# Kernel tuning notes

Hardware: AMD Instinct MI355X
Metric: run time of the kernel (lower is better)

The kernel has to match this reference:

```python
import jax, jax.numpy as jnp
import numpy as np

# MAML backbone parameter shapes (standard 4-conv few-shot net + 5-way logits head)
PARAM_SHAPES = [(64, 3, 3, 3), (64,), (64, 64, 3, 3), (64,), (64, 64, 3, 3), (64,),
                (64, 64, 3, 3), (64,), (5, 1600), (5,)]
GATE_DIM = 512   # hierarchicalClustering.input_dim + hidden_dim
B = 256          # meta-batch of tasks (vectorized over the original python loop)


def setup_inputs() -> dict:
    key = jax.random.key(0)
    ks = jax.random.split(key, 1 + 3 * len(PARAM_SHAPES))
    inp = {"emb": jax.random.normal(ks[0], (B, GATE_DIM), dtype=jnp.float32)}
    for i, s in enumerate(PARAM_SHAPES):
        n = int(np.prod(s))
        inp[f"p{i}"] = jax.random.normal(ks[1 + 3 * i], s, dtype=jnp.float32) * 0.05
        inp[f"W{i}"] = jax.random.normal(ks[2 + 3 * i], (n, GATE_DIM), dtype=jnp.float32) / np.float32(np.sqrt(GATE_DIM))
        inp[f"b{i}"] = jnp.zeros((n,), dtype=jnp.float32)
    return inp


def reference(emb, p0, W0, b0, p1, W1, b1, p2, W2, b2, p3, W3, b3, p4, W4, b4,
              p5, W5, b5, p6, W6, b6, p7, W7, b7, p8, W8, b8, p9, W9, b9):
    # Per MAML parameter tensor: eta = sigmoid(Linear(emb)); adapted = eta * theta.
    # Loop is over a small fixed set of structurally distinct params (10), vectorized over tasks B.
    triples = [(p0, W0, b0), (p1, W1, b1), (p2, W2, b2), (p3, W3, b3), (p4, W4, b4),
               (p5, W5, b5), (p6, W6, b6), (p7, W7, b7), (p8, W8, b8), (p9, W9, b9)]
    outs = []
    for p, W, b in triples:
        eta = jax.nn.sigmoid(emb @ W.T + b)          # [B, numel_i]
        outs.append(eta * p.reshape(-1))             # adapted theta_i, flattened
    return jnp.concatenate(outs, axis=1)             # [B, total_numel]
```

## Files before the change

kernel.cpp:

```cpp
#include <hip/hip_runtime.h>
#include <hip/hip_bf16.h>

#define GATE 512
#define MROWS 256
#define NTOT 120581

typedef __attribute__((ext_vector_type(8))) short short8;
typedef __attribute__((ext_vector_type(4))) float  f32x4;

struct GemmParams {
    const float* W[10];
    const float* p[10];
    const float* bias[10];
};

__device__ __forceinline__ short bf16bits(float x) {
    __hip_bfloat16 h = __float2bfloat16(x);
    return *reinterpret_cast<short*>(&h);
}

__global__ void emb_to_bf16(const float* __restrict__ emb,
                            unsigned short* __restrict__ o) {
    int i = (blockIdx.x * blockDim.x + threadIdx.x) * 8;
    f32x4 a = *(const f32x4*)(emb + i);
    f32x4 b = *(const f32x4*)(emb + i + 4);
    short8 r;
#pragma unroll
    for (int j = 0; j < 4; ++j) { r[j] = bf16bits(a[j]); r[4 + j] = bf16bits(b[j]); }
    *(short8*)(o + i) = r;
}

__global__ __launch_bounds__(256, 4) void gate_gemm(GemmParams P,
                                                    const unsigned short* __restrict__ embw,
                                                    float* __restrict__ out)
{
    constexpr int kStarts[11] = {0, 1728, 1792, 38656, 38720, 75584,
                                 75648, 112512, 112576, 120576, 120581};
    __shared__ unsigned short Atile[2][MROWS * 32];

    const int t    = threadIdx.x;
    const int lane = t & 63;
    const int wave = t >> 6;
    const int lr   = lane & 15;
    const int lg   = lane >> 4;

    const int  n     = blockIdx.x * 64 + wave * 16 + lr;
    const bool valid = n < NTOT;
    const int  nc    = valid ? n : NTOT - 1;
    int tt = 0;
#pragma unroll
    for (int i = 1; i < 10; ++i) tt += (nc >= kStarts[i]);
    const int rr = nc - kStarts[tt];
    const float* wrow = P.W[tt] + (size_t)rr * GATE + lg * 8;
    const float pv = P.p[tt][rr];
    const float bv = P.bias[tt][rr];

    const int srow  = t >> 2;
    const int sslot = (t & 3) ^ ((t >> 3) & 3);
    const unsigned short* asrc = embw + (size_t)srow * GATE + sslot * 8;

    const int aslot = lg ^ ((lr >> 1) & 3);
    const int abase = lr * 32 + aslot * 8;

    f32x4 acc[16];
#pragma unroll
    for (int i = 0; i < 16; ++i) acc[i] = (f32x4){0.f, 0.f, 0.f, 0.f};

    auto stage = [&](int buf, int kb) {
#pragma unroll
        for (int i = 0; i < 4; ++i) {
            const unsigned short* src = asrc + (size_t)i * 64 * GATE + kb;
            unsigned short* dst = &Atile[buf][(size_t)(i * 256 + t) * 8];
            __builtin_amdgcn_global_load_lds(
                (const __attribute__((address_space(1))) void*)src,
                (__attribute__((address_space(3))) void*)dst, 16, 0, 0);
        }
    };

    stage(0, 0);
    f32x4 b0 = *(const f32x4*)(wrow);
    f32x4 b1 = *(const f32x4*)(wrow + 4);
    __syncthreads();

    int buf = 0;
#pragma unroll
    for (int ks = 0; ks < 16; ++ks) {
        f32x4 nb0, nb1;
        if (ks < 15) {
            stage(buf ^ 1, (ks + 1) * 32);
            nb0 = *(const f32x4*)(wrow + (ks + 1) * 32);
            nb1 = *(const f32x4*)(wrow + (ks + 1) * 32 + 4);
        }

        short8 bfrag;
#pragma unroll
        for (int j = 0; j < 4; ++j) {
            bfrag[j]     = bf16bits(b0[j]);
            bfrag[4 + j] = bf16bits(b1[j]);
        }

        const unsigned short* ab = &Atile[buf][abase];
#pragma unroll
        for (int mf = 0; mf < 16; ++mf) {
            short8 afrag = *(const short8*)(ab + mf * 512);
            acc[mf] = __builtin_amdgcn_mfma_f32_16x16x32_bf16(afrag, bfrag, acc[mf], 0, 0, 0);
        }

        __syncthreads();
        b0 = nb0; b1 = nb1;
        buf ^= 1;
    }

    if (valid) {
        float* ocol = out + n;
#pragma unroll
        for (int mf = 0; mf < 16; ++mf) {
            const int m0 = mf * 16 + lg * 4;
#pragma unroll
            for (int q = 0; q < 4; ++q) {
                float x   = acc[mf][q] + bv;
                float e   = __expf(-x);
                float eta = __builtin_amdgcn_rcpf(1.0f + e);
                ocol[(size_t)(m0 + q) * NTOT] = eta * pv;
            }
        }
    }
}

extern "C" void kernel_launch(void* const* d_in, const int* in_sizes, int n_in,
                              void* d_out, int out_size, void* d_ws, size_t ws_size,
                              hipStream_t stream) {
    const float* emb = (const float*)d_in[0];
    GemmParams P;
    for (int i = 0; i < 10; ++i) {
        P.p[i]    = (const float*)d_in[1 + 3 * i];
        P.W[i]    = (const float*)d_in[2 + 3 * i];
        P.bias[i] = (const float*)d_in[3 + 3 * i];
    }

    unsigned short* embw = (unsigned short*)d_ws;
    emb_to_bf16<<<(MROWS * GATE) / (256 * 8), 256, 0, stream>>>(emb, embw);

    int nblocks = (NTOT + 63) / 64;
    gate_gemm<<<nblocks, 256, 0, stream>>>(P, embw, (float*)d_out);
}
```

Baseline: 131.3 us.

## Tile waves 2x2 over M and N and stage K in 64-wide phases

Each wave now computes 128 rows by 32 columns instead of 256 rows by 16 columns. Every A fragment loaded from LDS feeds two MFMAs, which halves LDS reads per MFMA. The A staging loads a 64-wide K slab (two 32-wide sub-tiles) per phase with two barriers per phase, instead of double-buffering every 32-wide K step. The trade-off is that global-to-LDS loads are no longer overlapped with compute, since each phase waits at barriers after staging, and each wave now loads two W rows at a time.

```diff
diff --git a/kernel.cpp b/kernel.cpp
--- a/kernel.cpp
+++ b/kernel.cpp
@@ -36,92 +36,126 @@
 {
     constexpr int kStarts[11] = {0, 1728, 1792, 38656, 38720, 75584,
                                  75648, 112512, 112576, 120576, 120581};
-    __shared__ unsigned short Atile[2][MROWS * 32];
+    __shared__ unsigned short Atile[2][MROWS][32];
 
     const int t    = threadIdx.x;
     const int lane = t & 63;
     const int wave = t >> 6;
+    const int wm   = wave >> 1;
+    const int wn   = wave & 1;
     const int lr   = lane & 15;
     const int lg   = lane >> 4;
 
-    const int  n     = blockIdx.x * 64 + wave * 16 + lr;
-    const bool valid = n < NTOT;
-    const int  nc    = valid ? n : NTOT - 1;
-    int tt = 0;
+    const float* wrow[2];
+    float pv[2], bv[2];
+    bool  valid[2];
+    int   ncol[2];
 #pragma unroll
-    for (int i = 1; i < 10; ++i) tt += (nc >= kStarts[i]);
-    const int rr = nc - kStarts[tt];
-    const float* wrow = P.W[tt] + (size_t)rr * GATE + lg * 8;
-    const float pv = P.p[tt][rr];
-    const float bv = P.bias[tt][rr];
+    for (int nf = 0; nf < 2; ++nf) {
+        int n  = blockIdx.x * 64 + wn * 32 + nf * 16 + lr;
+        ncol[nf]  = n;
+        valid[nf] = n < NTOT;
+        int nc = valid[nf] ? n : NTOT - 1;
+        int tt = 0;
+#pragma unroll
+        for (int i = 1; i < 10; ++i) tt += (nc >= kStarts[i]);
+        int r = nc - kStarts[tt];
+        wrow[nf] = P.W[tt] + (size_t)r * GATE + lg * 8;
+        pv[nf]   = P.p[tt][r];
+        bv[nf]   = P.bias[tt][r];
+    }
 
-    const int srow  = t >> 2;
+    const int srow0 = t >> 2;
     const int sslot = (t & 3) ^ ((t >> 3) & 3);
-    const unsigned short* asrc = embw + (size_t)srow * GATE + sslot * 8;
+    const unsigned short* asrc = embw + (size_t)srow0 * GATE + sslot * 8;
+    unsigned short* sdst = &Atile[0][0][0] + (size_t)t * 8;
+
+    auto stage = [&](int ph) {
+#pragma unroll
+        for (int sub = 0; sub < 2; ++sub)
+#pragma unroll
+            for (int i = 0; i < 4; ++i) {
+                const unsigned short* src = asrc + (size_t)i * 64 * GATE + ph * 64 + sub * 32;
+                unsigned short* dst = sdst + sub * 8192 + i * 2048;
+                __builtin_amdgcn_global_load_lds(
+                    (const __attribute__((address_space(1))) void*)src,
+                    (__attribute__((address_space(3))) void*)dst, 16, 0, 0);
+            }
+    };
 
     const int aslot = lg ^ ((lr >> 1) & 3);
-    const int abase = lr * 32 + aslot * 8;
+    const int abase = (wm * 128 + lr) * 32 + aslot * 8;
 
-    f32x4 acc[16];
+    f32x4 acc[8][2];
 #pragma unroll
-    for (int i = 0; i < 16; ++i) acc[i] = (f32x4){0.f, 0.f, 0.f, 0.f};
+    for (int i = 0; i < 8; ++i)
+#pragma unroll
+        for (int j = 0; j < 2; ++j) acc[i][j] = (f32x4){0.f, 0.f, 0.f, 0.f};
 
-    auto stage = [&](int buf, int kb) {
+    f32x4 Bcur[2][2], Bnxt[2][2];
+    auto loadB = [&](f32x4 (&B)[2][2], int gks) {
 #pragma unroll
-        for (int i = 0; i < 4; ++i) {
-            const unsigned short* src = asrc + (size_t)i * 64 * GATE + kb;
-            unsigned short* dst = &Atile[buf][(size_t)(i * 256 + t) * 8];
-            __builtin_amdgcn_global_load_lds(
-                (const __attribute__((address_space(1))) void*)src,
-                (__attribute__((address_space(3))) void*)dst, 16, 0, 0);
+        for (int nf = 0; nf < 2; ++nf) {
+            B[nf][0] = *(const f32x4*)(wrow[nf] + gks * 32);
+            B[nf][1] = *(const f32x4*)(wrow[nf] + gks * 32 + 4);
         }
     };
 
-    stage(0, 0);
-    f32x4 b0 = *(const f32x4*)(wrow);
-    f32x4 b1 = *(const f32x4*)(wrow + 4);
+    stage(0);
+    loadB(Bcur, 0);
     __syncthreads();
 
-    int buf = 0;
+    for (int ph = 0; ph < 8; ++ph) {
 #pragma unroll
-    for (int ks = 0; ks < 16; ++ks) {
-        f32x4 nb0, nb1;
-        if (ks < 15) {
-            stage(buf ^ 1, (ks + 1) * 32);
-            nb0 = *(const f32x4*)(wrow + (ks + 1) * 32);
-            nb1 = *(const f32x4*)(wrow + (ks + 1) * 32 + 4);
+        for (int sub = 0; sub < 2; ++sub) {
+            const int gks = ph * 2 + sub;
+            if (gks < 15) loadB(Bnxt, gks + 1);
+
+            short8 bfrag[2];
+#pragma unroll
+            for (int nf = 0; nf < 2; ++nf)
+#pragma unroll
+                for (int j = 0; j < 4; ++j) {
+                    bfrag[nf][j]     = bf16bits(Bcur[nf][0][j]);
+                    bfrag[nf][4 + j] = bf16bits(Bcur[nf][1][j]);
+                }
+
+            const unsigned short* ab = &Atile[0][0][0] + sub * 8192 + abase;
+#pragma unroll
+            for (int mf = 0; mf < 8; ++mf) {
+                short8 afrag = *(const short8*)(ab + mf * 512);
+                acc[mf][0] = __builtin_amdgcn_mfma_f32_16x16x32_bf16(afrag, bfrag[0], acc[mf][0], 0, 0, 0);
+                acc[mf][1] = __builtin_amdgcn_mfma_f32_16x16x32_bf16(afrag, bfrag[1], acc[mf][1], 0, 0, 0);
+            }
+
+            if (gks < 15) {
+#pragma unroll
+                for (int nf = 0; nf < 2; ++nf) {
+                    Bcur[nf][0] = Bnxt[nf][0];
+                    Bcur[nf][1] = Bnxt[nf][1];
+                }
+            }
         }
-
-        short8 bfrag;
-#pragma unroll
-        for (int j = 0; j < 4; ++j) {
-            bfrag[j]     = bf16bits(b0[j]);
-            bfrag[4 + j] = bf16bits(b1[j]);
+        if (ph < 7) {
+            __syncthreads();
+            stage(ph + 1);
+            __syncthreads();
         }
-
-        const unsigned short* ab = &Atile[buf][abase];
-#pragma unroll
-        for (int mf = 0; mf < 16; ++mf) {
-            short8 afrag = *(const short8*)(ab + mf * 512);
-            acc[mf] = __builtin_amdgcn_mfma_f32_16x16x32_bf16(afrag, bfrag, acc[mf], 0, 0, 0);
-        }
-
-        __syncthreads();
-        b0 = nb0; b1 = nb1;
-        buf ^= 1;
     }
 
-    if (valid) {
-        float* ocol = out + n;
 #pragma unroll
-        for (int mf = 0; mf < 16; ++mf) {
-            const int m0 = mf * 16 + lg * 4;
+    for (int nf = 0; nf < 2; ++nf) {
+        if (!valid[nf]) continue;
+        float* ocol = out + ncol[nf];
+#pragma unroll
+        for (int mf = 0; mf < 8; ++mf) {
+            const int m0 = wm * 128 + mf * 16 + lg * 4;
 #pragma unroll
             for (int q = 0; q < 4; ++q) {
-                float x   = acc[mf][q] + bv;
+                float x   = acc[mf][nf][q] + bv[nf];
                 float e   = __expf(-x);
                 float eta = __builtin_amdgcn_rcpf(1.0f + e);
-                ocol[(size_t)(m0 + q) * NTOT] = eta * pv;
+                ocol[(size_t)(m0 + q) * NTOT] = eta * pv[nf];
             }
         }
     }
```

Result: slower. 148.6 us (+13.1%).

## Load A fragments directly from global memory and triple-buffer W loads

Applied to the files above, without the earlier changes.

Drops the LDS double-buffered staging of the bf16 embedding tile and its per-step __syncthreads. Each wave now reads its A fragments straight from global memory, relying on L1/L2 caching of the small 256x512 bf16 matrix. W loads are prefetched two steps ahead in a three-slot register ring, and the occupancy hint in launch_bounds is removed. The aim is to cut barrier stalls and LDS traffic, at the cost of more global/L1 load instructions per MFMA and possible latency exposure.

```diff
diff --git a/kernel.cpp b/kernel.cpp
--- a/kernel.cpp
+++ b/kernel.cpp
@@ -30,13 +30,12 @@
     *(short8*)(o + i) = r;
 }
 
-__global__ __launch_bounds__(256, 4) void gate_gemm(GemmParams P,
-                                                    const unsigned short* __restrict__ embw,
-                                                    float* __restrict__ out)
+__global__ __launch_bounds__(256) void gate_gemm(GemmParams P,
+                                                 const unsigned short* __restrict__ embw,
+                                                 float* __restrict__ out)
 {
     constexpr int kStarts[11] = {0, 1728, 1792, 38656, 38720, 75584,
                                  75648, 112512, 112576, 120576, 120581};
-    __shared__ unsigned short Atile[2][MROWS * 32];
 
     const int t    = threadIdx.x;
     const int lane = t & 63;
@@ -55,60 +54,46 @@
     const float pv = P.p[tt][rr];
     const float bv = P.bias[tt][rr];
 
-    const int srow  = t >> 2;
-    const int sslot = (t & 3) ^ ((t >> 3) & 3);
-    const unsigned short* asrc = embw + (size_t)srow * GATE + sslot * 8;
-
-    const int aslot = lg ^ ((lr >> 1) & 3);
-    const int abase = lr * 32 + aslot * 8;
+    const unsigned short* arow = embw + lr * GATE + lg * 8;
 
     f32x4 acc[16];
 #pragma unroll
     for (int i = 0; i < 16; ++i) acc[i] = (f32x4){0.f, 0.f, 0.f, 0.f};
 
-    auto stage = [&](int buf, int kb) {
-#pragma unroll
-        for (int i = 0; i < 4; ++i) {
-            const unsigned short* src = asrc + (size_t)i * 64 * GATE + kb;
-            unsigned short* dst = &Atile[buf][(size_t)(i * 256 + t) * 8];
-            __builtin_amdgcn_global_load_lds(
-                (const __attribute__((address_space(1))) void*)src,
-                (__attribute__((address_space(3))) void*)dst, 16, 0, 0);
-        }
+    f32x4 Bbuf[3][2];
+    auto loadB = [&](f32x4 (&B)[2], int ks) {
+        B[0] = *(const f32x4*)(wrow + ks * 32);
+        B[1] = *(const f32x4*)(wrow + ks * 32 + 4);
     };
 
-    stage(0, 0);
-    f32x4 b0 = *(const f32x4*)(wrow);
-    f32x4 b1 = *(const f32x4*)(wrow + 4);
-    __syncthreads();
+    loadB(Bbuf[0], 0);
+    loadB(Bbuf[1], 1);
 
-    int buf = 0;
 #pragma unroll
     for (int ks = 0; ks < 16; ++ks) {
-        f32x4 nb0, nb1;
-        if (ks < 15) {
-            stage(buf ^ 1, (ks + 1) * 32);
-            nb0 = *(const f32x4*)(wrow + (ks + 1) * 32);
-            nb1 = *(const f32x4*)(wrow + (ks + 1) * 32 + 4);
-        }
+        if (ks + 2 < 16) loadB(Bbuf[(ks + 2) % 3], ks + 2);
 
         short8 bfrag;
 #pragma unroll
         for (int j = 0; j < 4; ++j) {
-            bfrag[j]     = bf16bits(b0[j]);
-            bfrag[4 + j] = bf16bits(b1[j]);
+            bfrag[j]     = bf16bits(Bbuf[ks % 3][0][j]);
+            bfrag[4 + j] = bf16bits(Bbuf[ks % 3][1][j]);
         }
 
-        const unsigned short* ab = &Atile[buf][abase];
+        short8 af[8];
 #pragma unroll
-        for (int mf = 0; mf < 16; ++mf) {
-            short8 afrag = *(const short8*)(ab + mf * 512);
-            acc[mf] = __builtin_amdgcn_mfma_f32_16x16x32_bf16(afrag, bfrag, acc[mf], 0, 0, 0);
-        }
+        for (int mf = 0; mf < 8; ++mf)
+            af[mf] = *(const short8*)(arow + mf * 16 * GATE + ks * 32);
+#pragma unroll
+        for (int mf = 0; mf < 8; ++mf)
+            acc[mf] = __builtin_amdgcn_mfma_f32_16x16x32_bf16(af[mf], bfrag, acc[mf], 0, 0, 0);
 
-        __syncthreads();
-        b0 = nb0; b1 = nb1;
-        buf ^= 1;
+#pragma unroll
+        for (int mf = 0; mf < 8; ++mf)
+            af[mf] = *(const short8*)(arow + (mf + 8) * 16 * GATE + ks * 32);
+#pragma unroll
+        for (int mf = 0; mf < 8; ++mf)
+            acc[mf + 8] = __builtin_amdgcn_mfma_f32_16x16x32_bf16(af[mf], bfrag, acc[mf + 8], 0, 0, 0);
     }
 
     if (valid) {
```

After: 317.1 us, median of 2. 2.41x slower.

## Double K-step per pipeline phase to halve barriers and deepen W prefetch

Applied to the files above, without the earlier changes.

Each pipeline phase now stages a 64-wide K slab of the bf16 embedding into LDS instead of 32, with an 8-slot XOR swizzle. Two 16x16x32 MFMA passes run per phase, so there are 8 barriers instead of 16, and each thread prefetches two K-steps of fp32 W ahead. The LDS footprint doubles to 64 KB and the occupancy hint of 4 blocks per SM is dropped. This can lower occupancy and raise register pressure from the extra prefetch buffers.

```diff
diff --git a/kernel.cpp b/kernel.cpp
--- a/kernel.cpp
+++ b/kernel.cpp
@@ -4,6 +4,7 @@
 #define GATE 512
 #define MROWS 256
 #define NTOT 120581
+#define PHK 64
 
 typedef __attribute__((ext_vector_type(8))) short short8;
 typedef __attribute__((ext_vector_type(4))) float  f32x4;
@@ -30,13 +31,13 @@
     *(short8*)(o + i) = r;
 }
 
-__global__ __launch_bounds__(256, 4) void gate_gemm(GemmParams P,
-                                                    const unsigned short* __restrict__ embw,
-                                                    float* __restrict__ out)
+__global__ __launch_bounds__(256) void gate_gemm(GemmParams P,
+                                                 const unsigned short* __restrict__ embw,
+                                                 float* __restrict__ out)
 {
     constexpr int kStarts[11] = {0, 1728, 1792, 38656, 38720, 75584,
                                  75648, 112512, 112576, 120576, 120581};
-    __shared__ unsigned short Atile[2][MROWS * 32];
+    __shared__ unsigned short Atile[2][MROWS * PHK];
 
     const int t    = threadIdx.x;
     const int lane = t & 63;
@@ -55,21 +56,14 @@
     const float pv = P.p[tt][rr];
     const float bv = P.bias[tt][rr];
 
-    const int srow  = t >> 2;
-    const int sslot = (t & 3) ^ ((t >> 3) & 3);
-    const unsigned short* asrc = embw + (size_t)srow * GATE + sslot * 8;
+    const int srow0 = t >> 3;
+    const int sslot = (t & 7) ^ ((t >> 3) & 7);
+    const unsigned short* asrc0 = embw + (size_t)srow0 * GATE + sslot * 8;
 
-    const int aslot = lg ^ ((lr >> 1) & 3);
-    const int abase = lr * 32 + aslot * 8;
-
-    f32x4 acc[16];
+    auto stage = [&](int buf, int p) {
 #pragma unroll
-    for (int i = 0; i < 16; ++i) acc[i] = (f32x4){0.f, 0.f, 0.f, 0.f};
-
-    auto stage = [&](int buf, int kb) {
-#pragma unroll
-        for (int i = 0; i < 4; ++i) {
-            const unsigned short* src = asrc + (size_t)i * 64 * GATE + kb;
+        for (int i = 0; i < 8; ++i) {
+            const unsigned short* src = asrc0 + (size_t)i * 32 * GATE + p * PHK;
             unsigned short* dst = &Atile[buf][(size_t)(i * 256 + t) * 8];
             __builtin_amdgcn_global_load_lds(
                 (const __attribute__((address_space(1))) void*)src,
@@ -77,38 +71,59 @@
         }
     };
 
+    const int axor = lr & 7;
+
+    f32x4 acc[16];
+#pragma unroll
+    for (int i = 0; i < 16; ++i) acc[i] = (f32x4){0.f, 0.f, 0.f, 0.f};
+
+    f32x4 Bc0[2], Bc1[2];
+    auto loadB = [&](f32x4 (&B)[2], int gks) {
+        B[0] = *(const f32x4*)(wrow + gks * 32);
+        B[1] = *(const f32x4*)(wrow + gks * 32 + 4);
+    };
+
     stage(0, 0);
-    f32x4 b0 = *(const f32x4*)(wrow);
-    f32x4 b1 = *(const f32x4*)(wrow + 4);
+    loadB(Bc0, 0);
+    loadB(Bc1, 1);
     __syncthreads();
 
     int buf = 0;
 #pragma unroll
-    for (int ks = 0; ks < 16; ++ks) {
-        f32x4 nb0, nb1;
-        if (ks < 15) {
-            stage(buf ^ 1, (ks + 1) * 32);
-            nb0 = *(const f32x4*)(wrow + (ks + 1) * 32);
-            nb1 = *(const f32x4*)(wrow + (ks + 1) * 32 + 4);
+    for (int p = 0; p < 8; ++p) {
+        f32x4 Bn0[2], Bn1[2];
+        if (p < 7) {
+            stage(buf ^ 1, p + 1);
+            loadB(Bn0, (p + 1) * 2);
+            loadB(Bn1, (p + 1) * 2 + 1);
         }
 
-        short8 bfrag;
+        short8 bf0;
 #pragma unroll
-        for (int j = 0; j < 4; ++j) {
-            bfrag[j]     = bf16bits(b0[j]);
-            bfrag[4 + j] = bf16bits(b1[j]);
+        for (int j = 0; j < 4; ++j) { bf0[j] = bf16bits(Bc0[0][j]); bf0[4 + j] = bf16bits(Bc0[1][j]); }
+#pragma unroll
+        for (int mf = 0; mf < 16; ++mf) {
+            const int idx = (mf * 16 + lr) * 64 + ((lg) ^ axor) * 8;
+            short8 af = *(const short8*)(&Atile[buf][idx]);
+            acc[mf] = __builtin_amdgcn_mfma_f32_16x16x32_bf16(af, bf0, acc[mf], 0, 0, 0);
         }
 
-        const unsigned short* ab = &Atile[buf][abase];
+        short8 bf1;
+#pragma unroll
+        for (int j = 0; j < 4; ++j) { bf1[j] = bf16bits(Bc1[0][j]); bf1[4 + j] = bf16bits(Bc1[1][j]); }
 #pragma unroll
         for (int mf = 0; mf < 16; ++mf) {
-            short8 afrag = *(const short8*)(ab + mf * 512);
-            acc[mf] = __builtin_amdgcn_mfma_f32_16x16x32_bf16(afrag, bfrag, acc[mf], 0, 0, 0);
+            const int idx = (mf * 16 + lr) * 64 + ((4 + lg) ^ axor) * 8;
+            short8 af = *(const short8*)(&Atile[buf][idx]);
+            acc[mf] = __builtin_amdgcn_mfma_f32_16x16x32_bf16(af, bf1, acc[mf], 0, 0, 0);
         }
 
-        __syncthreads();
-        b0 = nb0; b1 = nb1;
-        buf ^= 1;
+        if (p < 7) {
+#pragma unroll
+            for (int j = 0; j < 2; ++j) { Bc0[j] = Bn0[j]; Bc1[j] = Bn1[j]; }
+            __syncthreads();
+            buf ^= 1;
+        }
     }
 
     if (valid) {
```

Result: faster. 116.2 us (-11.5%).
